# Optimization experiments

Hardware: AMD Instinct MI355X
Metric: run time of the kernel (lower is better)

The kernel has to match this reference:

```python
import jax, jax.numpy as jnp
import numpy as np

NUM_FEATS = 3
CAT_SIZES = [10000, 8000, 100, 80]          # user, item, genre, year
CAT_TOTAL = sum(CAT_SIZES)                   # 18180
INPUT_DIM = NUM_FEATS + CAT_TOTAL            # 18183
EMB_DIM = 16
BATCH = 8192
CAT_OFFSETS = np.concatenate([[0], np.cumsum(CAT_SIZES)[:-1]])  # [0,10000,18000,18100]


def setup_inputs() -> dict:
    key = jax.random.key(0)
    k1, k2, k3, k4, k5, k6 = jax.random.split(key, 6)
    x_num = jax.random.normal(k1, (BATCH, NUM_FEATS), dtype=jnp.float32)
    x_cat = jax.random.randint(k2, (BATCH, len(CAT_SIZES)), 0, 80).astype(jnp.int64)
    v = 0.01 * jax.random.normal(k3, (INPUT_DIM, EMB_DIM), dtype=jnp.float32)
    global_bias = jax.random.uniform(k4, (1,), dtype=jnp.float32)
    num_bias = jax.random.uniform(k5, (NUM_FEATS,), dtype=jnp.float32)
    # per-feature nn.Embedding(size,1) tables, concatenated along the offset axis
    cat_bias = 0.01 * jax.random.normal(k6, (CAT_TOTAL,), dtype=jnp.float32)
    return {"x_num": x_num, "x_cat": x_cat, "v": v,
            "global_bias": global_bias, "num_bias": num_bias, "cat_bias": cat_bias}


def reference(x_num, x_cat, v, global_bias, num_bias, cat_bias):
    B = x_num.shape[0]
    offsets = jnp.asarray(CAT_OFFSETS, dtype=x_cat.dtype)
    idx = x_cat + offsets                                   # (B, n_cat), global ids
    # bias term: global + numeric linear + categorical embedding(size,1) lookups
    bias_term = (global_bias[0]
                 + jnp.sum(x_num * num_bias, axis=-1)
                 + jnp.sum(cat_bias[idx], axis=-1))          # (B,)
    # dense one-hot scatter (faithful to torch scatter_)
    onehot = jnp.zeros((B, CAT_TOTAL), dtype=x_num.dtype)
    onehot = onehot.at[jnp.arange(B)[:, None], idx].set(1.0)
    x_fm = jnp.concatenate([x_num, onehot], axis=1)          # (B, INPUT_DIM)
    # FM bilinear: 0.5 * sum( (xV)^2 - x^2 V^2 )
    square_of_sum = jnp.square(x_fm @ v)                     # (B, EMB_DIM)
    sum_of_square = jnp.square(x_fm) @ jnp.square(v)         # (B, EMB_DIM)
    y = bias_term + 0.5 * jnp.sum(square_of_sum - sum_of_square, axis=1)
    return y[:, None]                                        # (B, 1)
```

## Files before the change

kernel.cpp:

```cpp
#include <hip/hip_runtime.h>


#define FM_BATCH 8192
#define FM_EMB   16

__global__ __launch_bounds__(64) void fm_fwd_kernel(
    const float* __restrict__ x_num,
    const int*   __restrict__ x_cat,
    const float* __restrict__ v,
    const float* __restrict__ gbias,
    const float* __restrict__ nbias,
    const float* __restrict__ cbias,
    float*       __restrict__ out)
{
    const int b = blockIdx.x * blockDim.x + threadIdx.x;
    if (b >= FM_BATCH) return;

    const float xn0 = x_num[b * 3 + 0];
    const float xn1 = x_num[b * 3 + 1];
    const float xn2 = x_num[b * 3 + 2];

    const int i0 = x_cat[b * 4 + 0];
    const int i1 = x_cat[b * 4 + 1] + 10000;
    const int i2 = x_cat[b * 4 + 2] + 18000;
    const int i3 = x_cat[b * 4 + 3] + 18100;

    float bias = gbias[0]
               + xn0 * nbias[0] + xn1 * nbias[1] + xn2 * nbias[2]
               + cbias[i0] + cbias[i1] + cbias[i2] + cbias[i3];

    const float4* __restrict__ v4 = reinterpret_cast<const float4*>(v);
    const long r0 = (long)(3 + i0) * 4;
    const long r1 = (long)(3 + i1) * 4;
    const long r2 = (long)(3 + i2) * 4;
    const long r3 = (long)(3 + i3) * 4;

    float acc = 0.0f;
#pragma unroll
    for (int q = 0; q < 4; ++q) {
        const float4 a0 = v4[0 * 4 + q];
        const float4 a1 = v4[1 * 4 + q];
        const float4 a2 = v4[2 * 4 + q];
        const float4 c0 = v4[r0 + q];
        const float4 c1 = v4[r1 + q];
        const float4 c2 = v4[r2 + q];
        const float4 c3 = v4[r3 + q];

#define FM_COMP(f)                                                          \
        {                                                                   \
            const float t0 = xn0 * a0.f, t1 = xn1 * a1.f, t2 = xn2 * a2.f;  \
            const float s  = t0 + t1 + t2 + c0.f + c1.f + c2.f + c3.f;      \
            const float ss = t0 * t0 + t1 * t1 + t2 * t2                    \
                           + c0.f * c0.f + c1.f * c1.f                      \
                           + c2.f * c2.f + c3.f * c3.f;                     \
            acc += s * s - ss;                                              \
        }
        FM_COMP(x)
        FM_COMP(y)
        FM_COMP(z)
        FM_COMP(w)
#undef FM_COMP
    }

    out[b] = bias + 0.5f * acc;
}

extern "C" void kernel_launch(void* const* d_in, const int* in_sizes, int n_in,
                              void* d_out, int out_size, void* d_ws, size_t ws_size,
                              hipStream_t stream)
{
    const float* x_num = (const float*)d_in[0];
    const int*   x_cat = (const int*)  d_in[1];
    const float* v     = (const float*)d_in[2];
    const float* gb    = (const float*)d_in[3];
    const float* nb    = (const float*)d_in[4];
    const float* cb    = (const float*)d_in[5];
    float*       out   = (float*)d_out;

    const int block = 64;
    const int grid  = (FM_BATCH + block - 1) / block;
    fm_fwd_kernel<<<grid, block, 0, stream>>>(x_num, x_cat, v, gb, nb, cb, out);
}
```

Before: 64.65 us.

## Split each batch row across 16 lanes, one per embedding dim, with shuffle reduction

Assigns 16 threads per batch row, each handling one embedding dimension, and reduces the FM partial sums with xor shuffles. This turns the per-thread scattered float4 gathers into coalesced 64-byte row reads across a lane group and raises parallelism from 8192 to 131072 threads. In exchange each lane reloads x_num and x_cat redundantly, and a shuffle reduction is added.

```diff
diff --git a/kernel.cpp b/kernel.cpp
--- a/kernel.cpp
+++ b/kernel.cpp
@@ -2,9 +2,8 @@
 
 
 #define FM_BATCH 8192
-#define FM_EMB   16
 
-__global__ __launch_bounds__(64) void fm_fwd_kernel(
+__global__ __launch_bounds__(256) void fm_fwd_kernel(
     const float* __restrict__ x_num,
     const int*   __restrict__ x_cat,
     const float* __restrict__ v,
@@ -13,7 +12,9 @@
     const float* __restrict__ cbias,
     float*       __restrict__ out)
 {
-    const int b = blockIdx.x * blockDim.x + threadIdx.x;
+    const int tid = blockIdx.x * blockDim.x + threadIdx.x;
+    const int b = tid >> 4;
+    const int e = tid & 15;
     if (b >= FM_BATCH) return;
 
     const float xn0 = x_num[b * 3 + 0];
@@ -25,44 +26,31 @@
     const int i2 = x_cat[b * 4 + 2] + 18000;
     const int i3 = x_cat[b * 4 + 3] + 18100;
 
-    float bias = gbias[0]
-               + xn0 * nbias[0] + xn1 * nbias[1] + xn2 * nbias[2]
-               + cbias[i0] + cbias[i1] + cbias[i2] + cbias[i3];
+    const float a0 = v[0 * 16 + e];
+    const float a1 = v[1 * 16 + e];
+    const float a2 = v[2 * 16 + e];
+    const float c0 = v[(long)(3 + i0) * 16 + e];
+    const float c1 = v[(long)(3 + i1) * 16 + e];
+    const float c2 = v[(long)(3 + i2) * 16 + e];
+    const float c3 = v[(long)(3 + i3) * 16 + e];
 
-    const float4* __restrict__ v4 = reinterpret_cast<const float4*>(v);
-    const long r0 = (long)(3 + i0) * 4;
-    const long r1 = (long)(3 + i1) * 4;
-    const long r2 = (long)(3 + i2) * 4;
-    const long r3 = (long)(3 + i3) * 4;
+    const float t0 = xn0 * a0, t1 = xn1 * a1, t2 = xn2 * a2;
+    const float s  = t0 + t1 + t2 + c0 + c1 + c2 + c3;
+    const float ss = t0 * t0 + t1 * t1 + t2 * t2
+                   + c0 * c0 + c1 * c1 + c2 * c2 + c3 * c3;
+    float part = s * s - ss;
 
-    float acc = 0.0f;
-#pragma unroll
-    for (int q = 0; q < 4; ++q) {
-        const float4 a0 = v4[0 * 4 + q];
-        const float4 a1 = v4[1 * 4 + q];
-        const float4 a2 = v4[2 * 4 + q];
-        const float4 c0 = v4[r0 + q];
-        const float4 c1 = v4[r1 + q];
-        const float4 c2 = v4[r2 + q];
-        const float4 c3 = v4[r3 + q];
+    part += __shfl_xor(part, 1, 64);
+    part += __shfl_xor(part, 2, 64);
+    part += __shfl_xor(part, 4, 64);
+    part += __shfl_xor(part, 8, 64);
 
-#define FM_COMP(f)                                                          \
-        {                                                                   \
-            const float t0 = xn0 * a0.f, t1 = xn1 * a1.f, t2 = xn2 * a2.f;  \
-            const float s  = t0 + t1 + t2 + c0.f + c1.f + c2.f + c3.f;      \
-            const float ss = t0 * t0 + t1 * t1 + t2 * t2                    \
-                           + c0.f * c0.f + c1.f * c1.f                      \
-                           + c2.f * c2.f + c3.f * c3.f;                     \
-            acc += s * s - ss;                                              \
-        }
-        FM_COMP(x)
-        FM_COMP(y)
-        FM_COMP(z)
-        FM_COMP(w)
-#undef FM_COMP
+    if (e == 0) {
+        const float bias = gbias[0]
+                         + xn0 * nbias[0] + xn1 * nbias[1] + xn2 * nbias[2]
+                         + cbias[i0] + cbias[i1] + cbias[i2] + cbias[i3];
+        out[b] = bias + 0.5f * part;
     }
-
-    out[b] = bias + 0.5f * acc;
 }
 
 extern "C" void kernel_launch(void* const* d_in, const int* in_sizes, int n_in,
@@ -77,7 +65,8 @@
     const float* cb    = (const float*)d_in[5];
     float*       out   = (float*)d_out;
 
-    const int block = 64;
-    const int grid  = (FM_BATCH + block - 1) / block;
+    const int threads = FM_BATCH * 16;
+    const int block   = 256;
+    const int grid    = (threads + block - 1) / block;
     fm_fwd_kernel<<<grid, block, 0, stream>>>(x_num, x_cat, v, gb, nb, cb, out);
 }
```

Result: no change. 64.44 us (-0.3%).
